# Performance work log

Measured on AMD Instinct MI355X. Metric: run time of the kernel, lower is better.

Reference implementation:

```python
import jax, jax.numpy as jnp
import numpy as np

WH, WW = 7, 7
DIM, HEADS = 256, 8


def make_table_index(wh, ww):
    # relative coords table (log-spaced CPB input) and relative position index
    ch = np.arange(-(wh - 1), wh, dtype=np.float32)
    cw = np.arange(-(ww - 1), ww, dtype=np.float32)
    t = np.stack(np.meshgrid(ch, cw, indexing='ij'), axis=-1)[None]  # [1,2wh-1,2ww-1,2]
    t = t.copy()
    t[..., 0] /= (wh - 1)
    t[..., 1] /= (ww - 1)
    t *= 8.0
    t = np.sign(t) * np.log2(np.abs(t) + 1.0) / np.log2(8.0)
    coords = np.stack(np.meshgrid(np.arange(wh), np.arange(ww), indexing='ij'))
    cf = coords.reshape(2, -1)
    rc = (cf[:, :, None] - cf[:, None, :]).transpose(1, 2, 0).copy()  # [N,N,2]
    rc[..., 0] += wh - 1
    rc[..., 1] += ww - 1
    rc[..., 0] *= 2 * ww - 1
    idx = rc.sum(-1)
    return t.astype(np.float32), idx.astype(np.int32)


def setup_inputs() -> dict:
    key = jax.random.key(0)
    ks = jax.random.split(key, 10)
    B_, N, C, H = 2048, WH * WW, DIM, HEADS
    table, idx = make_table_index(WH, WW)
    return {
        'x': jax.random.normal(ks[0], (B_, N, C), jnp.float32),
        'mask': jnp.zeros((64, N, N), jnp.float32),
        'qkv_w': jax.random.normal(ks[1], (3 * C, C), jnp.float32) * 0.02,
        'q_bias': jnp.zeros((C,), jnp.float32),
        'v_bias': jnp.zeros((C,), jnp.float32),
        'logit_scale': jnp.full((H, 1, 1), np.log(10.0), jnp.float32),
        'cpb_w1': jax.random.normal(ks[2], (512, 2), jnp.float32) * 0.02,
        'cpb_b1': jnp.zeros((512,), jnp.float32),
        'cpb_w2': jax.random.normal(ks[3], (H, 512), jnp.float32) * 0.02,
        'proj_w': jax.random.normal(ks[4], (C, C), jnp.float32) * 0.02,
        'proj_b': jnp.zeros((C,), jnp.float32),
        'rel_coords_table': jnp.asarray(table),
        'rel_pos_index': jnp.asarray(idx),
    }


def _l2norm(t):
    return t / jnp.maximum(jnp.linalg.norm(t, axis=-1, keepdims=True), 1e-12)


def reference(x, mask, qkv_w, q_bias, v_bias, logit_scale, cpb_w1, cpb_b1,
              cpb_w2, proj_w, proj_b, rel_coords_table, rel_pos_index):
    B_, N, C = x.shape
    H = logit_scale.shape[0]
    hd = C // H
    qkv_b = jnp.concatenate([q_bias, jnp.zeros_like(v_bias), v_bias])
    qkv = (x @ qkv_w.T + qkv_b).reshape(B_, N, 3, H, hd).transpose(2, 0, 3, 1, 4)
    q, k, v = qkv[0], qkv[1], qkv[2]  # [B_,H,N,hd]
    attn = jnp.einsum('bhnd,bhmd->bhnm', _l2norm(q), _l2norm(k))
    scale = jnp.exp(jnp.minimum(logit_scale, jnp.log(jnp.float32(100.0))))  # [H,1,1]
    attn = attn * scale[None]
    # CPB MLP -> relative position bias
    table = jax.nn.relu(rel_coords_table @ cpb_w1.T + cpb_b1) @ cpb_w2.T  # [1,Th,Tw,H]
    table = table.reshape(-1, H)
    bias = table[rel_pos_index.reshape(-1)].reshape(N, N, H).transpose(2, 0, 1)
    attn = attn + 16.0 * jax.nn.sigmoid(bias)[None]
    nW = mask.shape[0]
    attn = attn.reshape(B_ // nW, nW, H, N, N) + mask[None, :, None]
    attn = jax.nn.softmax(attn.reshape(B_, H, N, N), axis=-1)
    out = jnp.einsum('bhnm,bhmd->bhnd', attn, v).transpose(0, 2, 1, 3).reshape(B_, N, C)
    return out @ proj_w.T + proj_b
```

## Files before the change

### kernel.cpp

```cpp
#include <hip/hip_runtime.h>

#define DEV __device__ __forceinline__

typedef float  f32x4  __attribute__((ext_vector_type(4)));
typedef __bf16 bf16x4 __attribute__((ext_vector_type(4)));
typedef __bf16 bf16x8 __attribute__((ext_vector_type(8)));

DEV unsigned short f2bf(float f) {
  unsigned u = __float_as_uint(f);
  u += 0x7fffu + ((u >> 16) & 1u);
  return (unsigned short)(u >> 16);
}

DEV void cp16(const void* g, void* l) {
  __builtin_amdgcn_global_load_lds((const __attribute__((address_space(1))) void*)g,
                                   (__attribute__((address_space(3))) void*)l, 16, 0, 0);
}

__global__ __launch_bounds__(256) void prep_kernel(
    const float* __restrict__ qkv_w, const float* __restrict__ proj_w,
    const float* __restrict__ q_bias, const float* __restrict__ v_bias,
    unsigned short* __restrict__ wq, unsigned short* __restrict__ wp,
    float* __restrict__ qkvb)
{
  int gid = blockIdx.x * 256 + threadIdx.x;
  if (gid < 196608) wq[gid] = f2bf(qkv_w[gid]);
  else              wp[gid - 196608] = f2bf(proj_w[gid - 196608]);
  if (gid < 768)
    qkvb[gid] = (gid < 256) ? q_bias[gid] : ((gid < 512) ? 0.f : v_bias[gid - 512]);
}

__global__ __launch_bounds__(256) void xbf16(
    const float* __restrict__ X, unsigned short* __restrict__ Xb)
{
  size_t gid = (size_t)blockIdx.x * 256 + threadIdx.x;
  const float4* xp = (const float4*)X;
  float4 f0 = xp[2 * gid], f1 = xp[2 * gid + 1];
  bf16x8 u;
  u[0] = (__bf16)f0.x; u[1] = (__bf16)f0.y; u[2] = (__bf16)f0.z; u[3] = (__bf16)f0.w;
  u[4] = (__bf16)f1.x; u[5] = (__bf16)f1.y; u[6] = (__bf16)f1.z; u[7] = (__bf16)f1.w;
  ((bf16x8*)Xb)[gid] = u;
}

__global__ __launch_bounds__(64) void cpb_mlp(
    const float* __restrict__ tab, const float* __restrict__ w1,
    const float* __restrict__ b1, const float* __restrict__ w2,
    float* __restrict__ table16)
{
  int r = blockIdx.x;
  int t = threadIdx.x;
  float x0 = tab[r * 2 + 0], x1 = tab[r * 2 + 1];
  float part[8];
#pragma unroll
  for (int h = 0; h < 8; ++h) part[h] = 0.f;
  for (int j = t; j < 512; j += 64) {
    float hv = fmaxf(w1[j * 2 + 0] * x0 + w1[j * 2 + 1] * x1 + b1[j], 0.f);
#pragma unroll
    for (int h = 0; h < 8; ++h) part[h] += hv * w2[h * 512 + j];
  }
#pragma unroll
  for (int h = 0; h < 8; ++h) {
    float v = part[h];
    for (int off = 32; off > 0; off >>= 1) v += __shfl_down(v, off, 64);
    if (t == 0) table16[r * 8 + h] = 16.f / (1.f + expf(-v));
  }
}

__global__ __launch_bounds__(256) void bmb(
    const float* __restrict__ t16, const int* __restrict__ ridx,
    const float* __restrict__ mask, float* __restrict__ bias64,
    float* __restrict__ mask64)
{
  const float L2E = 1.44269504f;
  int gid = blockIdx.x * 256 + threadIdx.x;
  int p = gid & 4095, i = p >> 6, j = p & 63;
  bool valid = (i < 49) && (j < 49);
  if (gid < 32768) {
    int h = gid >> 12;
    bias64[gid] = valid ? t16[ridx[i * 49 + j] * 8 + h] * L2E : -1e30f;
  } else {
    int g2 = gid - 32768;
    int w = g2 >> 12;
    mask64[g2] = valid ? mask[w * 2401 + i * 49 + j] * L2E : 0.f;
  }
}

__global__ __launch_bounds__(256) void gemm_qkv(
    const unsigned short* __restrict__ Xb, const unsigned short* __restrict__ W,
    const float* __restrict__ bias, unsigned short* __restrict__ qkv)
{
  __shared__ __align__(1024) unsigned short sA[128 * 64];
  __shared__ __align__(1024) unsigned short sB[128 * 64];
  const int t = threadIdx.x, w = t >> 6, l = t & 63, quad = l >> 4, l15 = l & 15;
  const int idx = blockIdx.x;
  const int x8 = idx & 7, local = idx >> 3;
  const int my = x8 * 98 + local / 6, bnb = local % 6;
  const int bm = my * 128, bn = bnb * 128;
  const int wm = (w >> 1) * 64, wn = (w & 1) * 64;
  const int srow = t >> 3, sch = t & 7;
  const int sc = sch ^ (srow & 7);

  const unsigned short* asrc = Xb + (size_t)(bm + srow) * 256 + sc * 8;
  const unsigned short* wsrc = W  + (size_t)(bn + srow) * 256 + sc * 8;

  f32x4 acc[4][4] = {};
  for (int kt = 0; kt < 4; ++kt) {
    const int k0 = kt << 6;
    if (kt) __syncthreads();
#pragma unroll
    for (int i = 0; i < 4; ++i) {
      cp16(asrc + (size_t)i * 32 * 256 + k0, sA + (i * 256 + w * 64) * 8);
      cp16(wsrc + (size_t)i * 32 * 256 + k0, sB + (i * 256 + w * 64) * 8);
    }
    __syncthreads();
#pragma unroll
    for (int kk = 0; kk < 2; ++kk) {
      bf16x8 xf[4], wf[4];
#pragma unroll
      for (int mt = 0; mt < 4; ++mt)
        xf[mt] = *(const bf16x8*)&sA[(wm + mt * 16 + l15) * 64 + (((4 * kk + quad) ^ (l15 & 7)) * 8)];
#pragma unroll
      for (int nt = 0; nt < 4; ++nt)
        wf[nt] = *(const bf16x8*)&sB[(wn + nt * 16 + l15) * 64 + (((4 * kk + quad) ^ (l15 & 7)) * 8)];
#pragma unroll
      for (int nt = 0; nt < 4; ++nt)
#pragma unroll
        for (int mt = 0; mt < 4; ++mt)
          acc[nt][mt] = __builtin_amdgcn_mfma_f32_16x16x32_bf16(wf[nt], xf[mt], acc[nt][mt], 0, 0, 0);
    }
  }
  const int nbase = bn + wn;
#pragma unroll
  for (int mA = 0; mA < 4; ++mA) {
    const int mrow = bm + wm + mA * 16 + l15;
    const unsigned bb = (unsigned)(((unsigned long long)mrow * 87652394ull) >> 32);
    const int tok = mrow - (int)bb * 49;
#pragma unroll
    for (int k = 0; k < 2; ++k) {
      const int n0 = nbase + k * 32;
      const int s = n0 >> 8, h = (n0 >> 5) & 7;
      const f32x4 b0 = *(const f32x4*)(bias + n0 + quad * 4);
      const f32x4 b1 = *(const f32x4*)(bias + n0 + 16 + quad * 4);
      const f32x4 a0 = acc[2 * k][mA], a1 = acc[2 * k + 1][mA];
      bf16x8 u;
      u[0] = (__bf16)(a0[0] + b0[0]); u[1] = (__bf16)(a0[1] + b0[1]);
      u[2] = (__bf16)(a0[2] + b0[2]); u[3] = (__bf16)(a0[3] + b0[3]);
      u[4] = (__bf16)(a1[0] + b1[0]); u[5] = (__bf16)(a1[1] + b1[1]);
      u[6] = (__bf16)(a1[2] + b1[2]); u[7] = (__bf16)(a1[3] + b1[3]);
      *(bf16x8*)(qkv + (size_t)((bb * 8u + h) * 3u + s) * 1568 + tok * 32 + quad * 8) = u;
    }
  }
}

__global__ __launch_bounds__(256) void attn2(
    const unsigned short* __restrict__ qkv, const float* __restrict__ logit_scale,
    const float* __restrict__ bias64, const float* __restrict__ mask64,
    unsigned short* __restrict__ aout)
{
  __shared__ __align__(1024) char smem[4 * 8192];
  const int w = threadIdx.x >> 6, l = threadIdx.x & 63, quad = l >> 4, l15 = l & 15;
  const int flat = blockIdx.x * 4 + w;
  const int b = flat >> 3, h = flat & 7;
  unsigned short* P = (unsigned short*)(smem + w * 8192);

  const unsigned short* qb = qkv + (size_t)flat * 4704;
  const unsigned short* kb = qb + 1568;
  const unsigned short* vb = qb + 3136;

  bf16x8 kf[4], qf[4];
#pragma unroll
  for (int mt = 0; mt < 4; ++mt) kf[mt] = *(const bf16x8*)(kb + (mt * 16 + l15) * 32 + quad * 8);
#pragma unroll
  for (int nt = 0; nt < 4; ++nt) qf[nt] = *(const bf16x8*)(qb + (nt * 16 + l15) * 32 + quad * 8);

  const float scale = __expf(fminf(logit_scale[h], 4.60517019f)) * 1.44269504f;
  float rqv[4];
#pragma unroll
  for (int nt = 0; nt < 4; ++nt) {
    float s = 0.f;
#pragma unroll
    for (int d = 0; d < 8; ++d) { float f = (float)qf[nt][d]; s += f * f; }
    s += __shfl_xor(s, 16, 64); s += __shfl_xor(s, 32, 64);
    rqv[nt] = scale / fmaxf(sqrtf(s), 1e-12f);
  }
  float rkl[4];
#pragma unroll
  for (int mt = 0; mt < 4; ++mt) {
    float s = 0.f;
#pragma unroll
    for (int d = 0; d < 8; ++d) { float f = (float)kf[mt][d]; s += f * f; }
    s += __shfl_xor(s, 16, 64); s += __shfl_xor(s, 32, 64);
    rkl[mt] = 1.f / fmaxf(sqrtf(s), 1e-12f);
  }
  f32x4 rk4v[4];
#pragma unroll
  for (int mt = 0; mt < 4; ++mt)
#pragma unroll
    for (int r = 0; r < 4; ++r)
      rk4v[mt][r] = __shfl(rkl[mt], (quad << 2) + r, 16);

  f32x4 acc[4][4] = {};
  __builtin_amdgcn_s_setprio(1);
#pragma unroll
  for (int mt = 0; mt < 4; ++mt)
#pragma unroll
    for (int nt = 0; nt < 4; ++nt)
      acc[mt][nt] = __builtin_amdgcn_mfma_f32_16x16x32_bf16(kf[mt], qf[nt], acc[mt][nt], 0, 0, 0);
  __builtin_amdgcn_s_setprio(0);

  const float* bh = bias64 + (size_t)h * 4096;
  const float* mw = mask64 + (size_t)(b & 63) * 4096;
  float rs4[4];
#pragma unroll
  for (int nt = 0; nt < 4; ++nt) {
    const int i = nt * 16 + l15;
    const float rqi = rqv[nt];
    float mx = -3e38f;
#pragma unroll
    for (int mt = 0; mt < 4; ++mt) {
      const int jb = mt * 16 + quad * 4;
      const f32x4 b4 = *(const f32x4*)(bh + i * 64 + jb);
      const f32x4 m4 = *(const f32x4*)(mw + i * 64 + jb);
#pragma unroll
      for (int r = 0; r < 4; ++r) {
        float sv = fmaf(acc[mt][nt][r], rqi * rk4v[mt][r], b4[r] + m4[r]);
        acc[mt][nt][r] = sv;
        mx = fmaxf(mx, sv);
      }
    }
    mx = fmaxf(mx, __shfl_xor(mx, 16, 64));
    mx = fmaxf(mx, __shfl_xor(mx, 32, 64));
    float sum = 0.f;
#pragma unroll
    for (int mt = 0; mt < 4; ++mt) {
      float pv[4];
#pragma unroll
      for (int r = 0; r < 4; ++r) {
        pv[r] = __builtin_amdgcn_exp2f(acc[mt][nt][r] - mx);
        sum += pv[r];
      }
      bf16x4 pk;
      pk[0] = (__bf16)pv[0]; pk[1] = (__bf16)pv[1];
      pk[2] = (__bf16)pv[2]; pk[3] = (__bf16)pv[3];
      const int c = 2 * mt + (quad >> 1);
      *(bf16x4*)((char*)P + i * 128 + ((c ^ (i & 7)) * 16) + (quad & 1) * 8) = pk;
    }
    sum += __shfl_xor(sum, 16, 64);
    sum += __shfl_xor(sum, 32, 64);
    rs4[nt] = 1.f / sum;
  }

  asm volatile("s_waitcnt lgkmcnt(0)" ::: "memory");

  f32x4 oacc[2][4] = {};
#pragma unroll
  for (int kk = 0; kk < 2; ++kk) {
    bf16x8 vf[2], pf[4];
#pragma unroll
    for (int mt = 0; mt < 2; ++mt) {
      const __bf16* vp = (const __bf16*)vb +
          (32 * kk + quad * 8) * 32 + (l15 >> 2) * 8 + mt * 4 + (l15 & 3);
#pragma unroll
      for (int s = 0; s < 8; ++s) vf[mt][s] = vp[s * 32];
    }
#pragma unroll
    for (int nt = 0; nt < 4; ++nt)
      pf[nt] = *(const bf16x8*)((char*)P + (nt * 16 + l15) * 128 + (((4 * kk + quad) ^ (l15 & 7)) * 16));
    __builtin_amdgcn_s_setprio(1);
#pragma unroll
    for (int mt = 0; mt < 2; ++mt)
#pragma unroll
      for (int nt = 0; nt < 4; ++nt)
        oacc[mt][nt] = __builtin_amdgcn_mfma_f32_16x16x32_bf16(vf[mt], pf[nt], oacc[mt][nt], 0, 0, 0);
    __builtin_amdgcn_s_setprio(0);
  }

#pragma unroll
  for (int nt = 0; nt < 4; ++nt) {
    const int tok = nt * 16 + l15;
    if (tok < 49) {
      unsigned short* op = aout + (size_t)(b * 49 + tok) * 256 + h * 32;
      const float rs = rs4[nt];
#pragma unroll
      for (int mt = 0; mt < 2; ++mt) {
        bf16x4 ov;
        ov[0] = (__bf16)(oacc[mt][nt][0] * rs); ov[1] = (__bf16)(oacc[mt][nt][1] * rs);
        ov[2] = (__bf16)(oacc[mt][nt][2] * rs); ov[3] = (__bf16)(oacc[mt][nt][3] * rs);
        *(bf16x4*)(op + mt * 16 + quad * 4) = ov;
      }
    }
  }
}

__global__ __launch_bounds__(256) void gemm_proj(
    const unsigned short* __restrict__ A, const unsigned short* __restrict__ W,
    const float* __restrict__ bias, float* __restrict__ Y)
{
  __shared__ __align__(1024) unsigned short sA[128 * 64];
  __shared__ __align__(1024) unsigned short sB[128 * 64];
  const int t = threadIdx.x, w = t >> 6, l = t & 63, quad = l >> 4, l15 = l & 15;
  const int bm = blockIdx.y * 128, bn = blockIdx.x * 128;
  const int wm = (w >> 1) * 64, wn = (w & 1) * 64;
  const int srow = t >> 3, sch = t & 7;
  const int sc = sch ^ (srow & 7);

  f32x4 acc[4][4] = {};
  for (int kt = 0; kt < 4; ++kt) {
    const int k0 = kt << 6;
    if (kt) __syncthreads();
#pragma unroll
    for (int i = 0; i < 4; ++i) {
      const int row = i * 32 + srow;
      cp16(A + (size_t)(bm + row) * 256 + k0 + sc * 8, sA + (i * 256 + w * 64) * 8);
      cp16(W + (size_t)(bn + row) * 256 + k0 + sc * 8, sB + (i * 256 + w * 64) * 8);
    }
    __syncthreads();
#pragma unroll
    for (int kk = 0; kk < 2; ++kk) {
      bf16x8 xf[4], wf[4];
#pragma unroll
      for (int mt = 0; mt < 4; ++mt)
        xf[mt] = *(const bf16x8*)&sA[(wm + mt * 16 + l15) * 64 + (((4 * kk + quad) ^ (l15 & 7)) * 8)];
#pragma unroll
      for (int nt = 0; nt < 4; ++nt)
        wf[nt] = *(const bf16x8*)&sB[(wn + nt * 16 + l15) * 64 + (((4 * kk + quad) ^ (l15 & 7)) * 8)];
#pragma unroll
      for (int nt = 0; nt < 4; ++nt)
#pragma unroll
        for (int mt = 0; mt < 4; ++mt)
          acc[nt][mt] = __builtin_amdgcn_mfma_f32_16x16x32_bf16(wf[nt], xf[mt], acc[nt][mt], 0, 0, 0);
    }
  }
#pragma unroll
  for (int mA = 0; mA < 4; ++mA) {
    const int row = bm + wm + mA * 16 + l15;
    float* orow = Y + (size_t)row * 256;
#pragma unroll
    for (int nW = 0; nW < 4; ++nW) {
      const int c0 = bn + wn + nW * 16 + quad * 4;
      const f32x4 bv = *(const f32x4*)(bias + c0);
      f32x4 v = acc[nW][mA];
      v[0] += bv[0]; v[1] += bv[1]; v[2] += bv[2]; v[3] += bv[3];
      *(f32x4*)(orow + c0) = v;
    }
  }
}

extern "C" void kernel_launch(void* const* d_in, const int* in_sizes, int n_in,
                              void* d_out, int out_size, void* d_ws, size_t ws_size,
                              hipStream_t stream) {
  const float* x           = (const float*)d_in[0];
  const float* mask        = (const float*)d_in[1];
  const float* qkv_w       = (const float*)d_in[2];
  const float* q_bias      = (const float*)d_in[3];
  const float* v_bias      = (const float*)d_in[4];
  const float* logit_scale = (const float*)d_in[5];
  const float* cpb_w1      = (const float*)d_in[6];
  const float* cpb_b1      = (const float*)d_in[7];
  const float* cpb_w2      = (const float*)d_in[8];
  const float* proj_w      = (const float*)d_in[9];
  const float* proj_b      = (const float*)d_in[10];
  const float* rel_tab     = (const float*)d_in[11];
  const int*   rel_idx     = (const int*)d_in[12];
  float*       out         = (float*)d_out;

  char* ws = (char*)d_ws;
  unsigned short* qkvp    = (unsigned short*)(ws + 0);
  unsigned short* aows    = (unsigned short*)(ws + 154140672);
  unsigned short* wq      = (unsigned short*)(ws + 205520896);
  unsigned short* wp      = (unsigned short*)(ws + 205914112);
  float*          qkvb    = (float*)(ws + 206045184);
  float*          table16 = (float*)(ws + 206048256);
  float*          bias64  = (float*)(ws + 206053888);
  float*          mask64  = (float*)(ws + 206184960);
  unsigned short* xbf = aows;

  prep_kernel<<<1024, 256, 0, stream>>>(qkv_w, proj_w, q_bias, v_bias, wq, wp, qkvb);
  cpb_mlp<<<169, 64, 0, stream>>>(rel_tab, cpb_w1, cpb_b1, cpb_w2, table16);
  bmb<<<1152, 256, 0, stream>>>(table16, rel_idx, mask, bias64, mask64);
  xbf16<<<12544, 256, 0, stream>>>(x, xbf);
  gemm_qkv<<<4704, 256, 0, stream>>>(xbf, wq, qkvb, qkvp);
  attn2<<<4096, 256, 0, stream>>>(qkvp, logit_scale, bias64, mask64, aows);
  gemm_proj<<<dim3(2, 784), 256, 0, stream>>>(aows, wp, proj_b, out);
}
```

Measured before the change: 409.6 us.

## Fuse QKV projection GEMM into per-window attention kernel

Replaces the separate QKV GEMM and attention kernels with one kernel per window. Each block stages the window's 49 token rows of bf16 x in LDS, computes the K, Q and V head slices with MFMA, and bounces them through per-wave LDS into fragment layout before running attention. This removes the round trip of the full QKV intermediate through global memory and one kernel launch. In exchange, weight fragments are read straight from global memory with no LDS reuse, rows are padded from 49 to 64, and LDS use grows to 64KB per block, which may reduce occupancy.

```diff
diff --git a/kernel.cpp b/kernel.cpp
--- a/kernel.cpp
+++ b/kernel.cpp
@@ -85,208 +85,236 @@
   }
 }
 
-__global__ __launch_bounds__(256) void gemm_qkv(
+__global__ __launch_bounds__(256) void qkv_attn(
     const unsigned short* __restrict__ Xb, const unsigned short* __restrict__ W,
-    const float* __restrict__ bias, unsigned short* __restrict__ qkv)
-{
-  __shared__ __align__(1024) unsigned short sA[128 * 64];
-  __shared__ __align__(1024) unsigned short sB[128 * 64];
-  const int t = threadIdx.x, w = t >> 6, l = t & 63, quad = l >> 4, l15 = l & 15;
-  const int idx = blockIdx.x;
-  const int x8 = idx & 7, local = idx >> 3;
-  const int my = x8 * 98 + local / 6, bnb = local % 6;
-  const int bm = my * 128, bn = bnb * 128;
-  const int wm = (w >> 1) * 64, wn = (w & 1) * 64;
-  const int srow = t >> 3, sch = t & 7;
-  const int sc = sch ^ (srow & 7);
-
-  const unsigned short* asrc = Xb + (size_t)(bm + srow) * 256 + sc * 8;
-  const unsigned short* wsrc = W  + (size_t)(bn + srow) * 256 + sc * 8;
-
-  f32x4 acc[4][4] = {};
-  for (int kt = 0; kt < 4; ++kt) {
-    const int k0 = kt << 6;
-    if (kt) __syncthreads();
-#pragma unroll
-    for (int i = 0; i < 4; ++i) {
-      cp16(asrc + (size_t)i * 32 * 256 + k0, sA + (i * 256 + w * 64) * 8);
-      cp16(wsrc + (size_t)i * 32 * 256 + k0, sB + (i * 256 + w * 64) * 8);
-    }
-    __syncthreads();
-#pragma unroll
-    for (int kk = 0; kk < 2; ++kk) {
-      bf16x8 xf[4], wf[4];
-#pragma unroll
-      for (int mt = 0; mt < 4; ++mt)
-        xf[mt] = *(const bf16x8*)&sA[(wm + mt * 16 + l15) * 64 + (((4 * kk + quad) ^ (l15 & 7)) * 8)];
-#pragma unroll
-      for (int nt = 0; nt < 4; ++nt)
-        wf[nt] = *(const bf16x8*)&sB[(wn + nt * 16 + l15) * 64 + (((4 * kk + quad) ^ (l15 & 7)) * 8)];
-#pragma unroll
-      for (int nt = 0; nt < 4; ++nt)
-#pragma unroll
-        for (int mt = 0; mt < 4; ++mt)
-          acc[nt][mt] = __builtin_amdgcn_mfma_f32_16x16x32_bf16(wf[nt], xf[mt], acc[nt][mt], 0, 0, 0);
-    }
-  }
-  const int nbase = bn + wn;
-#pragma unroll
-  for (int mA = 0; mA < 4; ++mA) {
-    const int mrow = bm + wm + mA * 16 + l15;
-    const unsigned bb = (unsigned)(((unsigned long long)mrow * 87652394ull) >> 32);
-    const int tok = mrow - (int)bb * 49;
-#pragma unroll
-    for (int k = 0; k < 2; ++k) {
-      const int n0 = nbase + k * 32;
-      const int s = n0 >> 8, h = (n0 >> 5) & 7;
-      const f32x4 b0 = *(const f32x4*)(bias + n0 + quad * 4);
-      const f32x4 b1 = *(const f32x4*)(bias + n0 + 16 + quad * 4);
-      const f32x4 a0 = acc[2 * k][mA], a1 = acc[2 * k + 1][mA];
-      bf16x8 u;
-      u[0] = (__bf16)(a0[0] + b0[0]); u[1] = (__bf16)(a0[1] + b0[1]);
-      u[2] = (__bf16)(a0[2] + b0[2]); u[3] = (__bf16)(a0[3] + b0[3]);
-      u[4] = (__bf16)(a1[0] + b1[0]); u[5] = (__bf16)(a1[1] + b1[1]);
-      u[6] = (__bf16)(a1[2] + b1[2]); u[7] = (__bf16)(a1[3] + b1[3]);
-      *(bf16x8*)(qkv + (size_t)((bb * 8u + h) * 3u + s) * 1568 + tok * 32 + quad * 8) = u;
-    }
-  }
-}
-
-__global__ __launch_bounds__(256) void attn2(
-    const unsigned short* __restrict__ qkv, const float* __restrict__ logit_scale,
+    const float* __restrict__ qkvb, const float* __restrict__ logit_scale,
     const float* __restrict__ bias64, const float* __restrict__ mask64,
     unsigned short* __restrict__ aout)
 {
-  __shared__ __align__(1024) char smem[4 * 8192];
-  const int w = threadIdx.x >> 6, l = threadIdx.x & 63, quad = l >> 4, l15 = l & 15;
-  const int flat = blockIdx.x * 4 + w;
-  const int b = flat >> 3, h = flat & 7;
-  unsigned short* P = (unsigned short*)(smem + w * 8192);
-
-  const unsigned short* qb = qkv + (size_t)flat * 4704;
-  const unsigned short* kb = qb + 1568;
-  const unsigned short* vb = qb + 3136;
-
-  bf16x8 kf[4], qf[4];
-#pragma unroll
-  for (int mt = 0; mt < 4; ++mt) kf[mt] = *(const bf16x8*)(kb + (mt * 16 + l15) * 32 + quad * 8);
-#pragma unroll
-  for (int nt = 0; nt < 4; ++nt) qf[nt] = *(const bf16x8*)(qb + (nt * 16 + l15) * 32 + quad * 8);
-
-  const float scale = __expf(fminf(logit_scale[h], 4.60517019f)) * 1.44269504f;
-  float rqv[4];
-#pragma unroll
-  for (int nt = 0; nt < 4; ++nt) {
-    float s = 0.f;
-#pragma unroll
-    for (int d = 0; d < 8; ++d) { float f = (float)qf[nt][d]; s += f * f; }
-    s += __shfl_xor(s, 16, 64); s += __shfl_xor(s, 32, 64);
-    rqv[nt] = scale / fmaxf(sqrtf(s), 1e-12f);
-  }
-  float rkl[4];
-#pragma unroll
-  for (int mt = 0; mt < 4; ++mt) {
-    float s = 0.f;
-#pragma unroll
-    for (int d = 0; d < 8; ++d) { float f = (float)kf[mt][d]; s += f * f; }
-    s += __shfl_xor(s, 16, 64); s += __shfl_xor(s, 32, 64);
-    rkl[mt] = 1.f / fmaxf(sqrtf(s), 1e-12f);
-  }
-  f32x4 rk4v[4];
-#pragma unroll
-  for (int mt = 0; mt < 4; ++mt)
-#pragma unroll
-    for (int r = 0; r < 4; ++r)
-      rk4v[mt][r] = __shfl(rkl[mt], (quad << 2) + r, 16);
-
-  f32x4 acc[4][4] = {};
-  __builtin_amdgcn_s_setprio(1);
-#pragma unroll
-  for (int mt = 0; mt < 4; ++mt)
-#pragma unroll
-    for (int nt = 0; nt < 4; ++nt)
-      acc[mt][nt] = __builtin_amdgcn_mfma_f32_16x16x32_bf16(kf[mt], qf[nt], acc[mt][nt], 0, 0, 0);
-  __builtin_amdgcn_s_setprio(0);
-
-  const float* bh = bias64 + (size_t)h * 4096;
-  const float* mw = mask64 + (size_t)(b & 63) * 4096;
-  float rs4[4];
-#pragma unroll
-  for (int nt = 0; nt < 4; ++nt) {
-    const int i = nt * 16 + l15;
-    const float rqi = rqv[nt];
-    float mx = -3e38f;
+  __shared__ __align__(1024) char smem[65536];
+  const int t = threadIdx.x, w = t >> 6, l = t & 63, quad = l >> 4, l15 = l & 15;
+  char* sX  = smem;
+  char* myr = smem + 32768 + w * 8192;
+
+  const int win = blockIdx.x;
+  const int wtok = win * 49;
+
+  {
+    const int r0 = w * 16;
+    const int s = l & 31;
+#pragma unroll
+    for (int i = 0; i < 8; ++i) {
+      const int row = r0 + 2 * i + (l >> 5);
+      if (row < 49) {
+        const unsigned short* src = Xb + (size_t)(wtok + row) * 256
+                                  + (s >> 3) * 64 + (((s & 7) ^ (row & 7)) * 8);
+        cp16(src, sX + (r0 + 2 * i) * 512);
+      } else {
+        uint4 z; z.x = z.y = z.z = z.w = 0u;
+        *(uint4*)(sX + row * 512 + s * 16) = z;
+      }
+    }
+  }
+  __syncthreads();
+
+  const int bslot = (quad ^ ((l15 >> 1) & 3)) * 16;
+
+  auto do_gemm = [&](int wrb, f32x4 (&acc)[2][4]) {
+#pragma unroll
+    for (int kt = 0; kt < 4; ++kt)
+#pragma unroll
+      for (int kk = 0; kk < 2; ++kk) {
+        bf16x8 wf[2], xf[4];
+#pragma unroll
+        for (int nt = 0; nt < 2; ++nt)
+          wf[nt] = *(const bf16x8*)(W + (size_t)(wrb + nt * 16 + l15) * 256
+                                      + kt * 64 + (4 * kk + quad) * 8);
+#pragma unroll
+        for (int mA = 0; mA < 4; ++mA)
+          xf[mA] = *(const bf16x8*)(sX + (mA * 16 + l15) * 512 + kt * 128
+                                       + (((4 * kk + quad) ^ (l15 & 7)) * 16));
+#pragma unroll
+        for (int nt = 0; nt < 2; ++nt)
+#pragma unroll
+          for (int mA = 0; mA < 4; ++mA)
+            acc[nt][mA] = __builtin_amdgcn_mfma_f32_16x16x32_bf16(wf[nt], xf[mA], acc[nt][mA], 0, 0, 0);
+      }
+  };
+
+  auto bounce = [&](f32x4 (&acc)[2][4], const float* bias, bf16x8 (&f)[4]) {
+    const f32x4 b0 = *(const f32x4*)(bias + quad * 4);
+    const f32x4 b1 = *(const f32x4*)(bias + 16 + quad * 4);
+#pragma unroll
+    for (int mA = 0; mA < 4; ++mA) {
+      bf16x8 u;
+      u[0] = (__bf16)(acc[0][mA][0] + b0[0]); u[1] = (__bf16)(acc[0][mA][1] + b0[1]);
+      u[2] = (__bf16)(acc[0][mA][2] + b0[2]); u[3] = (__bf16)(acc[0][mA][3] + b0[3]);
+      u[4] = (__bf16)(acc[1][mA][0] + b1[0]); u[5] = (__bf16)(acc[1][mA][1] + b1[1]);
+      u[6] = (__bf16)(acc[1][mA][2] + b1[2]); u[7] = (__bf16)(acc[1][mA][3] + b1[3]);
+      *(bf16x8*)(myr + (mA * 16 + l15) * 64 + bslot) = u;
+    }
+    asm volatile("s_waitcnt lgkmcnt(0)" ::: "memory");
+    __builtin_amdgcn_sched_barrier(0);
+#pragma unroll
+    for (int mt = 0; mt < 4; ++mt)
+      f[mt] = *(const bf16x8*)(myr + (mt * 16 + l15) * 64 + bslot);
+  };
+
+#pragma unroll 1
+  for (int hh = 0; hh < 2; ++hh) {
+    const int h = 2 * w + hh;
+
+    f32x4 ka[2][4] = {};
+    do_gemm(256 + h * 32, ka);
+    bf16x8 kf[4];
+    bounce(ka, qkvb + 256 + h * 32, kf);
+
+    f32x4 qa[2][4] = {};
+    do_gemm(h * 32, qa);
+    bf16x8 qf[4];
+    bounce(qa, qkvb + h * 32, qf);
+
+    const float scale = __expf(fminf(logit_scale[h], 4.60517019f)) * 1.44269504f;
+    float rqv[4];
+#pragma unroll
+    for (int nt = 0; nt < 4; ++nt) {
+      float s = 0.f;
+#pragma unroll
+      for (int d = 0; d < 8; ++d) { float f = (float)qf[nt][d]; s += f * f; }
+      s += __shfl_xor(s, 16, 64); s += __shfl_xor(s, 32, 64);
+      rqv[nt] = scale / fmaxf(sqrtf(s), 1e-12f);
+    }
+    float rkl[4];
 #pragma unroll
     for (int mt = 0; mt < 4; ++mt) {
-      const int jb = mt * 16 + quad * 4;
-      const f32x4 b4 = *(const f32x4*)(bh + i * 64 + jb);
-      const f32x4 m4 = *(const f32x4*)(mw + i * 64 + jb);
-#pragma unroll
-      for (int r = 0; r < 4; ++r) {
-        float sv = fmaf(acc[mt][nt][r], rqi * rk4v[mt][r], b4[r] + m4[r]);
-        acc[mt][nt][r] = sv;
-        mx = fmaxf(mx, sv);
-      }
-    }
-    mx = fmaxf(mx, __shfl_xor(mx, 16, 64));
-    mx = fmaxf(mx, __shfl_xor(mx, 32, 64));
-    float sum = 0.f;
-#pragma unroll
-    for (int mt = 0; mt < 4; ++mt) {
-      float pv[4];
-#pragma unroll
-      for (int r = 0; r < 4; ++r) {
-        pv[r] = __builtin_amdgcn_exp2f(acc[mt][nt][r] - mx);
-        sum += pv[r];
-      }
-      bf16x4 pk;
-      pk[0] = (__bf16)pv[0]; pk[1] = (__bf16)pv[1];
-      pk[2] = (__bf16)pv[2]; pk[3] = (__bf16)pv[3];
-      const int c = 2 * mt + (quad >> 1);
-      *(bf16x4*)((char*)P + i * 128 + ((c ^ (i & 7)) * 16) + (quad & 1) * 8) = pk;
-    }
-    sum += __shfl_xor(sum, 16, 64);
-    sum += __shfl_xor(sum, 32, 64);
-    rs4[nt] = 1.f / sum;
-  }
-
-  asm volatile("s_waitcnt lgkmcnt(0)" ::: "memory");
-
-  f32x4 oacc[2][4] = {};
-#pragma unroll
-  for (int kk = 0; kk < 2; ++kk) {
-    bf16x8 vf[2], pf[4];
-#pragma unroll
-    for (int mt = 0; mt < 2; ++mt) {
-      const __bf16* vp = (const __bf16*)vb +
-          (32 * kk + quad * 8) * 32 + (l15 >> 2) * 8 + mt * 4 + (l15 & 3);
-#pragma unroll
-      for (int s = 0; s < 8; ++s) vf[mt][s] = vp[s * 32];
-    }
-#pragma unroll
-    for (int nt = 0; nt < 4; ++nt)
-      pf[nt] = *(const bf16x8*)((char*)P + (nt * 16 + l15) * 128 + (((4 * kk + quad) ^ (l15 & 7)) * 16));
+      float s = 0.f;
+#pragma unroll
+      for (int d = 0; d < 8; ++d) { float f = (float)kf[mt][d]; s += f * f; }
+      s += __shfl_xor(s, 16, 64); s += __shfl_xor(s, 32, 64);
+      rkl[mt] = 1.f / fmaxf(sqrtf(s), 1e-12f);
+    }
+    f32x4 rk4v[4];
+#pragma unroll
+    for (int mt = 0; mt < 4; ++mt)
+#pragma unroll
+      for (int r = 0; r < 4; ++r)
+        rk4v[mt][r] = __shfl(rkl[mt], (quad << 2) + r, 16);
+
+    {
+      f32x4 va[2][4] = {};
+      do_gemm(512 + h * 32, va);
+      const f32x4 vb0 = *(const f32x4*)(qkvb + 512 + h * 32 + quad * 4);
+      const f32x4 vb1 = *(const f32x4*)(qkvb + 512 + h * 32 + 16 + quad * 4);
+#pragma unroll
+      for (int mA = 0; mA < 4; ++mA) {
+        const int tok = mA * 16 + l15;
+#pragma unroll
+        for (int nt = 0; nt < 2; ++nt) {
+#pragma unroll
+          for (int r = 0; r < 4; ++r) {
+            const int d = nt * 16 + quad * 4 + r;
+            *(__bf16*)(myr + d * 128 + (((tok >> 3) ^ (d & 7)) << 4) + (tok & 7) * 2) =
+                (__bf16)(va[nt][mA][r] + (nt ? vb1[r] : vb0[r]));
+          }
+        }
+      }
+    }
+    asm volatile("s_waitcnt lgkmcnt(0)" ::: "memory");
+    __builtin_amdgcn_sched_barrier(0);
+    bf16x8 vf[2][2];
+#pragma unroll
+    for (int kk = 0; kk < 2; ++kk)
+#pragma unroll
+      for (int mt = 0; mt < 2; ++mt)
+        vf[kk][mt] = *(const bf16x8*)(myr + (mt * 16 + l15) * 128
+                                          + (((4 * kk + quad) ^ (l15 & 7)) * 16));
+    asm volatile("s_waitcnt lgkmcnt(0)" ::: "memory");
+    __builtin_amdgcn_sched_barrier(0);
+
+    f32x4 sacc[4][4] = {};
     __builtin_amdgcn_s_setprio(1);
 #pragma unroll
-    for (int mt = 0; mt < 2; ++mt)
+    for (int mt = 0; mt < 4; ++mt)
 #pragma unroll
       for (int nt = 0; nt < 4; ++nt)
-        oacc[mt][nt] = __builtin_amdgcn_mfma_f32_16x16x32_bf16(vf[mt], pf[nt], oacc[mt][nt], 0, 0, 0);
+        sacc[mt][nt] = __builtin_amdgcn_mfma_f32_16x16x32_bf16(kf[mt], qf[nt], sacc[mt][nt], 0, 0, 0);
     __builtin_amdgcn_s_setprio(0);
-  }
-
-#pragma unroll
-  for (int nt = 0; nt < 4; ++nt) {
-    const int tok = nt * 16 + l15;
-    if (tok < 49) {
-      unsigned short* op = aout + (size_t)(b * 49 + tok) * 256 + h * 32;
-      const float rs = rs4[nt];
-#pragma unroll
-      for (int mt = 0; mt < 2; ++mt) {
-        bf16x4 ov;
-        ov[0] = (__bf16)(oacc[mt][nt][0] * rs); ov[1] = (__bf16)(oacc[mt][nt][1] * rs);
-        ov[2] = (__bf16)(oacc[mt][nt][2] * rs); ov[3] = (__bf16)(oacc[mt][nt][3] * rs);
-        *(bf16x4*)(op + mt * 16 + quad * 4) = ov;
+
+    unsigned short* P = (unsigned short*)myr;
+    const float* bh = bias64 + (size_t)h * 4096;
+    const float* mw = mask64 + (size_t)(win & 63) * 4096;
+    float rs4[4];
+#pragma unroll
+    for (int nt = 0; nt < 4; ++nt) {
+      const int i = nt * 16 + l15;
+      const float rqi = rqv[nt];
+      float mx = -3e38f;
+#pragma unroll
+      for (int mt = 0; mt < 4; ++mt) {
+        const int jb = mt * 16 + quad * 4;
+        const f32x4 b4 = *(const f32x4*)(bh + i * 64 + jb);
+        const f32x4 m4 = *(const f32x4*)(mw + i * 64 + jb);
+#pragma unroll
+        for (int r = 0; r < 4; ++r) {
+          float sv = fmaf(sacc[mt][nt][r], rqi * rk4v[mt][r], b4[r] + m4[r]);
+          sacc[mt][nt][r] = sv;
+          mx = fmaxf(mx, sv);
+        }
+      }
+      mx = fmaxf(mx, __shfl_xor(mx, 16, 64));
+      mx = fmaxf(mx, __shfl_xor(mx, 32, 64));
+      float sum = 0.f;
+#pragma unroll
+      for (int mt = 0; mt < 4; ++mt) {
+        float pv[4];
+#pragma unroll
+        for (int r = 0; r < 4; ++r) {
+          pv[r] = __builtin_amdgcn_exp2f(sacc[mt][nt][r] - mx);
+          sum += pv[r];
+        }
+        bf16x4 pk;
+        pk[0] = (__bf16)pv[0]; pk[1] = (__bf16)pv[1];
+        pk[2] = (__bf16)pv[2]; pk[3] = (__bf16)pv[3];
+        const int c = 2 * mt + (quad >> 1);
+        *(bf16x4*)((char*)P + i * 128 + ((c ^ (i & 7)) * 16) + (quad & 1) * 8) = pk;
+      }
+      sum += __shfl_xor(sum, 16, 64);
+      sum += __shfl_xor(sum, 32, 64);
+      rs4[nt] = 1.f / sum;
+    }
+    asm volatile("s_waitcnt lgkmcnt(0)" ::: "memory");
+    __builtin_amdgcn_sched_barrier(0);
+
+    f32x4 oacc[2][4] = {};
+#pragma unroll
+    for (int kk = 0; kk < 2; ++kk) {
+      bf16x8 pf[4];
+#pragma unroll
+      for (int nt = 0; nt < 4; ++nt)
+        pf[nt] = *(const bf16x8*)((char*)P + (nt * 16 + l15) * 128
+                                           + (((4 * kk + quad) ^ (l15 & 7)) * 16));
+      __builtin_amdgcn_s_setprio(1);
+#pragma unroll
+      for (int mt = 0; mt < 2; ++mt)
+#pragma unroll
+        for (int nt = 0; nt < 4; ++nt)
+          oacc[mt][nt] = __builtin_amdgcn_mfma_f32_16x16x32_bf16(vf[kk][mt], pf[nt], oacc[mt][nt], 0, 0, 0);
+      __builtin_amdgcn_s_setprio(0);
+    }
+
+#pragma unroll
+    for (int nt = 0; nt < 4; ++nt) {
+      const int tok = nt * 16 + l15;
+      if (tok < 49) {
+        unsigned short* op = aout + (size_t)(wtok + tok) * 256 + h * 32;
+        const float rs = rs4[nt];
+#pragma unroll
+        for (int mt = 0; mt < 2; ++mt) {
+          bf16x4 ov;
+          ov[0] = (__bf16)(oacc[mt][nt][0] * rs); ov[1] = (__bf16)(oacc[mt][nt][1] * rs);
+          ov[2] = (__bf16)(oacc[mt][nt][2] * rs); ov[3] = (__bf16)(oacc[mt][nt][3] * rs);
+          *(bf16x4*)(op + mt * 16 + quad * 4) = ov;
+        }
       }
     }
   }
@@ -365,7 +393,7 @@
   float*       out         = (float*)d_out;
 
   char* ws = (char*)d_ws;
-  unsigned short* qkvp    = (unsigned short*)(ws + 0);
+  unsigned short* xbf     = (unsigned short*)(ws + 0);
   unsigned short* aows    = (unsigned short*)(ws + 154140672);
   unsigned short* wq      = (unsigned short*)(ws + 205520896);
   unsigned short* wp      = (unsigned short*)(ws + 205914112);
@@ -373,13 +401,11 @@
   float*          table16 = (float*)(ws + 206048256);
   float*          bias64  = (float*)(ws + 206053888);
   float*          mask64  = (float*)(ws + 206184960);
-  unsigned short* xbf = aows;
 
   prep_kernel<<<1024, 256, 0, stream>>>(qkv_w, proj_w, q_bias, v_bias, wq, wp, qkvb);
   cpb_mlp<<<169, 64, 0, stream>>>(rel_tab, cpb_w1, cpb_b1, cpb_w2, table16);
   bmb<<<1152, 256, 0, stream>>>(table16, rel_idx, mask, bias64, mask64);
   xbf16<<<12544, 256, 0, stream>>>(x, xbf);
-  gemm_qkv<<<4704, 256, 0, stream>>>(xbf, wq, qkvb, qkvp);
-  attn2<<<4096, 256, 0, stream>>>(qkvp, logit_scale, bias64, mask64, aows);
+  qkv_attn<<<2048, 256, 0, stream>>>(xbf, wq, qkvb, logit_scale, bias64, mask64, aows);
   gemm_proj<<<dim3(2, 784), 256, 0, stream>>>(aows, wp, proj_b, out);
 }
```

Result: no change. 413.3 us (+0.9%).
